# Optimization experiments

Hardware: AMD Instinct MI355X
Metric: run time of the kernel (lower is better)

## Reference

```python
import math
import jax, jax.numpy as jnp
import numpy as np

V = 32000   # vocab_size
NL = 8      # n_layer
NH = 16     # n_head
D = 1024    # n_embd
DH = D // NH
FF = 4 * D
B = 2
L = 1024
EPS = 1e-5


def setup_inputs() -> dict:
    key = jax.random.key(0)
    ks = jax.random.split(key, 10)
    std = 0.02  # matches nn.init.normal_(std=0.02)
    def nrm(k, shape):
        return jax.random.normal(k, shape, jnp.float32) * std
    return {
        "idx": jax.random.randint(ks[0], (B, L), 0, V),
        "tok_emb": nrm(ks[1], (V, D)),
        # per-layer params stacked on leading NL axis (scanned over)
        "ln1_w": jnp.ones((NL, D)), "ln1_b": jnp.zeros((NL, D)),
        "wq": nrm(ks[2], (NL, D, D)), "wk": nrm(ks[3], (NL, D, D)),
        "wv": nrm(ks[4], (NL, D, D)), "wo": nrm(ks[5], (NL, D, D)),
        "ln2_w": jnp.ones((NL, D)), "ln2_b": jnp.zeros((NL, D)),
        "w1": nrm(ks[6], (NL, D, FF)), "b1": jnp.zeros((NL, FF)),
        "w2": nrm(ks[7], (NL, FF, D)), "b2": jnp.zeros((NL, D)),
        "lnf_w": jnp.ones((D,)), "lnf_b": jnp.zeros((D,)),
        "lm_head": nrm(ks[8], (D, V)),
    }


def _sinusoidal_pe(seq_len, dim):
    pos = jnp.arange(seq_len, dtype=jnp.float32)[:, None]
    div = jnp.exp(jnp.arange(0, dim, 2, dtype=jnp.float32) * (-math.log(10000.0) / dim))
    pe = jnp.zeros((seq_len, dim), jnp.float32)
    pe = pe.at[:, 0::2].set(jnp.sin(pos * div))
    pe = pe.at[:, 1::2].set(jnp.cos(pos * div))
    return pe


def _ln(x, w, b):
    m = x.mean(-1, keepdims=True)
    v = ((x - m) ** 2).mean(-1, keepdims=True)
    return (x - m) * jax.lax.rsqrt(v + EPS) * w + b


def reference(idx, tok_emb, ln1_w, ln1_b, wq, wk, wv, wo,
              ln2_w, ln2_b, w1, b1, w2, b2, lnf_w, lnf_b, lm_head):
    b, l = idx.shape
    x = tok_emb[idx] + _sinusoidal_pe(l, tok_emb.shape[1])[None]  # [B,L,D]
    causal = jnp.tril(jnp.ones((l, l), bool))
    scale = 1.0 / math.sqrt(DH)

    def block(x, p):
        l1w, l1b, Wq, Wk, Wv, Wo, l2w, l2b, W1, B1, W2, B2 = p
        h = _ln(x, l1w, l1b)
        def heads(W):  # [B,L,D] -> [B,H,L,DH]
            return (h @ W).reshape(b, l, NH, DH).transpose(0, 2, 1, 3)
        q, k, v = heads(Wq), heads(Wk), heads(Wv)
        att = jnp.einsum('bhqd,bhkd->bhqk', q, k) * scale
        att = jnp.where(causal, att, -jnp.inf)
        att = jax.nn.softmax(att, axis=-1)
        y = jnp.einsum('bhqk,bhkd->bhqd', att, v)
        y = y.transpose(0, 2, 1, 3).reshape(b, l, -1)
        x = x + y @ Wo
        h2 = _ln(x, l2w, l2b)
        x = x + jax.nn.gelu(h2 @ W1 + B1, approximate=False) @ W2 + B2
        return x, None

    x, _ = jax.lax.scan(
        block, x, (ln1_w, ln1_b, wq, wk, wv, wo, ln2_w, ln2_b, w1, b1, w2, b2))
    x = _ln(x, lnf_w, lnf_b)
    return x @ lm_head  # [B,L,V] logits
```

## Files before the change

### kernel.cpp

```cpp
#include <hip/hip_runtime.h>
#include <math.h>

typedef unsigned short u16;
typedef __bf16 bfx8 __attribute__((ext_vector_type(8)));
typedef float f32x4 __attribute__((ext_vector_type(4)));

#define NLAYER  8
#define NHEAD   16
#define DMODEL  1024
#define DHEAD   64
#define DFF     4096
#define NB      2
#define SEQ     1024
#define NVOCAB  32000
#define NTOK    (NB*SEQ)
#define EPSLN   1e-5f
#define VCHUNK  6400
#define NSPLIT  2

__device__ __forceinline__ float bf2f(u16 u) {
  union { unsigned int i; float f; } x; x.i = ((unsigned int)u) << 16; return x.f;
}
__device__ __forceinline__ u16 f2bf(float f) {
  unsigned int x = __float_as_uint(f);
  x += 0x7fffu + ((x >> 16) & 1u);
  return (u16)(x >> 16);
}

#if defined(__has_builtin)
#if __has_builtin(__builtin_amdgcn_global_load_lds)
#define HAVE_GLL 1
#endif
#endif

__device__ __forceinline__ void gll16(const void* g, void* lds_base, int lane) {
#ifdef HAVE_GLL
  __builtin_amdgcn_global_load_lds((const __attribute__((address_space(1))) unsigned int*)g,
                                   (__attribute__((address_space(3))) unsigned int*)lds_base,
                                   16, 0, 0);
  (void)lane;
#else
  *(uint4*)((char*)lds_base + lane * 16) = *(const uint4*)g;
#endif
}

enum { EPI_QKV = 0, EPI_GELU_BIAS = 1, EPI_RESID = 2, EPI_RESID_BIAS = 3, EPI_LOGITS = 4 };

template <int EPI, int BM>
__global__ __launch_bounds__(256) void gemm_bt(
    const u16* __restrict__ A, const u16* __restrict__ Bt,
    const float* __restrict__ bias, u16* __restrict__ outb,
    float* __restrict__ outf, int M, int N, int K, int ldc)
{
  constexpr int ARND = BM / 64;
  constexpr int MF = BM / 32;
  constexpr int ABYTES = BM * 32 * 2;
  constexpr int BBYTES = 128 * 32 * 2;
  __shared__ __align__(16) u16 sA[2][BM * 32];
  __shared__ __align__(16) u16 sB[2][128 * 32];

  const int tid  = threadIdx.x;
  const int w    = tid >> 6;
  const int lane = tid & 63;
  const int l16  = lane & 15;
  const int hi   = lane >> 4;
  const int wm   = w >> 1;
  const int wn   = w & 1;

  const int nwg = gridDim.x;
  const int MB  = M / BM;
  const int orig = blockIdx.x;
  const int xcd = orig & 7, li = orig >> 3;
  const int q = nwg >> 3, r = nwg & 7;
  const int work = (xcd < r ? xcd * (q + 1) : r * (q + 1) + (xcd - r) * q) + li;
  const int m0 = (work % MB) * BM;
  const int n0 = (work / MB) * 128;

  const int srow = lane >> 2;
  const int su   = lane & 3;

  const u16* gA[ARND]; const u16* gB[2];
  int laOff[ARND]; int lbOff[2];
#pragma unroll
  for (int r2 = 0; r2 < ARND; r2++) {
    const int row = r2 * 64 + w * 16 + srow;
    const int gu = su ^ ((row >> 1) & 3);
    gA[r2] = A + (size_t)(m0 + row) * K + gu * 8;
    laOff[r2] = (r2 * 64 + w * 16) * 64;
  }
#pragma unroll
  for (int r2 = 0; r2 < 2; r2++) {
    const int row = r2 * 64 + w * 16 + srow;
    const int gu = su ^ ((row >> 1) & 3);
    gB[r2] = Bt + (size_t)(n0 + row) * K + gu * 8;
    lbOff[r2] = (r2 * 64 + w * 16) * 64;
  }

  f32x4 acc[MF][4];
#pragma unroll
  for (int i = 0; i < MF; i++)
#pragma unroll
    for (int j = 0; j < 4; j++)
#pragma unroll
      for (int r2 = 0; r2 < 4; r2++) acc[i][j][r2] = 0.0f;

#pragma unroll
  for (int r2 = 0; r2 < ARND; r2++) { gll16(gA[r2], (char*)sA[0] + laOff[r2], lane); gA[r2] += 32; }
#pragma unroll
  for (int r2 = 0; r2 < 2; r2++)    { gll16(gB[r2], (char*)sB[0] + lbOff[r2], lane); gB[r2] += 32; }
  __syncthreads();

  const int NT = K >> 5;
  int cur = 0;
  for (int t = 0; t < NT; ++t) {
    if (t + 1 < NT) {
      char* nA = (char*)sA[0] + (cur ^ 1) * ABYTES;
      char* nB = (char*)sB[0] + (cur ^ 1) * BBYTES;
#pragma unroll
      for (int r2 = 0; r2 < ARND; r2++) { gll16(gA[r2], nA + laOff[r2], lane); gA[r2] += 32; }
#pragma unroll
      for (int r2 = 0; r2 < 2; r2++)    { gll16(gB[r2], nB + lbOff[r2], lane); gB[r2] += 32; }
    }

    const char* cA = (const char*)sA[0] + cur * ABYTES;
    const char* cB = (const char*)sB[0] + cur * BBYTES;
    bfx8 aF[MF], bF[4];
#pragma unroll
    for (int i = 0; i < MF; i++) {
      const int row = wm * (BM / 2) + i * 16 + l16;
      aF[i] = *(const bfx8*)(cA + row * 64 + ((hi ^ ((row >> 1) & 3)) << 4));
    }
#pragma unroll
    for (int j = 0; j < 4; j++) {
      const int row = wn * 64 + j * 16 + l16;
      bF[j] = *(const bfx8*)(cB + row * 64 + ((hi ^ ((row >> 1) & 3)) << 4));
    }
#pragma unroll
    for (int i = 0; i < MF; i++)
#pragma unroll
      for (int j = 0; j < 4; j++)
        acc[i][j] = __builtin_amdgcn_mfma_f32_16x16x32_bf16(aF[i], bF[j], acc[i][j], 0, 0, 0);
    __syncthreads();
    cur ^= 1;
  }

  const int rbase = m0 + wm * (BM / 2);
  const int cbase = n0 + wn * 64;
#pragma unroll
  for (int i = 0; i < MF; i++) {
#pragma unroll
    for (int j = 0; j < 4; j++) {
      const int gcol = cbase + j * 16 + l16;
      float bv = 0.0f;
      if constexpr (EPI == EPI_GELU_BIAS || EPI == EPI_RESID_BIAS) bv = bias[gcol];
#pragma unroll
      for (int r2 = 0; r2 < 4; r2++) {
        const int grow = rbase + i * 16 + hi * 4 + r2;
        float v = acc[i][j][r2];
        const size_t oi = (size_t)grow * ldc + gcol;
        if constexpr (EPI == EPI_QKV) {
          outb[oi] = f2bf(v);
        } else if constexpr (EPI == EPI_GELU_BIAS) {
          v += bv;
          v = 0.5f * v * (1.0f + erff(v * 0.70710678118654752f));
          outb[oi] = f2bf(v);
        } else if constexpr (EPI == EPI_RESID) {
          outf[oi] += v;
        } else if constexpr (EPI == EPI_RESID_BIAS) {
          outf[oi] += v + bv;
        } else {
          outf[oi] = v;
        }
      }
    }
  }
}

__global__ __launch_bounds__(256) void ln_kernel(
    const float* __restrict__ x, const float* __restrict__ w,
    const float* __restrict__ b, u16* __restrict__ out)
{
  const int row = blockIdx.x;
  const int tid = threadIdx.x;
  const float* xr = x + (size_t)row * DMODEL;
  float4 v = *(const float4*)(xr + tid * 4);
  __shared__ float sbuf[4], qbuf[4];
  float s = v.x + v.y + v.z + v.w;
  float ss = v.x * v.x + v.y * v.y + v.z * v.z + v.w * v.w;
#pragma unroll
  for (int o = 32; o > 0; o >>= 1) { s += __shfl_xor(s, o, 64); ss += __shfl_xor(ss, o, 64); }
  if ((tid & 63) == 0) { sbuf[tid >> 6] = s; qbuf[tid >> 6] = ss; }
  __syncthreads();
  const float mean = (sbuf[0] + sbuf[1] + sbuf[2] + sbuf[3]) * (1.0f / DMODEL);
  const float ex2  = (qbuf[0] + qbuf[1] + qbuf[2] + qbuf[3]) * (1.0f / DMODEL);
  const float rstd = rsqrtf(ex2 - mean * mean + EPSLN);
  const int c = tid * 4;
  float dv[4] = {v.x - mean, v.y - mean, v.z - mean, v.w - mean};
#pragma unroll
  for (int e = 0; e < 4; e++)
    out[(size_t)row * DMODEL + c + e] = f2bf(dv[e] * rstd * w[c + e] + b[c + e]);
}

__global__ __launch_bounds__(256) void embed_kernel(
    const int* __restrict__ idx, const float* __restrict__ tok, float* __restrict__ x)
{
  const int row = blockIdx.x;
  const int l = row & (SEQ - 1);
  const int t = idx[row];
  const int d = threadIdx.x * 4;
#pragma unroll
  for (int e = 0; e < 4; e++) {
    const int dd = d + e;
    const float freq = expf((float)(dd & ~1) * (-9.210340371976184f / (float)DMODEL));
    const float ang = (float)l * freq;
    const float pe = (dd & 1) ? cosf(ang) : sinf(ang);
    x[(size_t)row * DMODEL + dd] = tok[(size_t)t * DMODEL + dd] + pe;
  }
}

__device__ __forceinline__ void transpose64_body(
    const float* __restrict__ in, u16* __restrict__ out,
    int rows, int cols, int c0, int r0)
{
  __shared__ float tile[64][65];
  const int lx = threadIdx.x & 15, ly = threadIdx.x >> 4;
#pragma unroll
  for (int ii = 0; ii < 4; ii++) {
    const int rr = ly + ii * 16;
    const float4 v = *(const float4*)&in[(size_t)(r0 + rr) * cols + c0 + lx * 4];
    tile[rr][lx * 4 + 0] = v.x;
    tile[rr][lx * 4 + 1] = v.y;
    tile[rr][lx * 4 + 2] = v.z;
    tile[rr][lx * 4 + 3] = v.w;
  }
  __syncthreads();
  const int sx = threadIdx.x & 31, sy = threadIdx.x >> 5;
#pragma unroll
  for (int ii = 0; ii < 8; ii++) {
    const int cc = sy + ii * 8;
    const unsigned int a = f2bf(tile[sx * 2][cc]);
    const unsigned int b = f2bf(tile[sx * 2 + 1][cc]);
    *(unsigned int*)&out[(size_t)(c0 + cc) * rows + r0 + sx * 2] = a | (b << 16);
  }
}

__global__ __launch_bounds__(256) void transpose64_b(
    const float* __restrict__ in, u16* __restrict__ out, int rows, int cols)
{
  transpose64_body(in, out, rows, cols, blockIdx.x * 64, blockIdx.y * 64);
}

__global__ __launch_bounds__(256) void transpose6_kernel(
    const float* __restrict__ wq, const float* __restrict__ wk,
    const float* __restrict__ wv, const float* __restrict__ wo,
    const float* __restrict__ w1, const float* __restrict__ w2,
    u16* __restrict__ wT)
{
  const size_t dd = (size_t)DMODEL * DMODEL, dff = (size_t)DMODEL * DFF;
  const int t = blockIdx.x;
  const float* in; u16* out; int rows, cols, cx, cy;
  if (t < 1024) {
    const int mat = t >> 8, tl = t & 255;
    in = (mat == 0) ? wq : (mat == 1) ? wk : (mat == 2) ? wv : wo;
    out = wT + (size_t)mat * dd; rows = DMODEL; cols = DMODEL;
    cx = tl & 15; cy = tl >> 4;
  } else if (t < 2048) {
    const int tl = t - 1024;
    in = w1; out = wT + 4 * dd; rows = DMODEL; cols = DFF;
    cx = tl & 63; cy = tl >> 6;
  } else {
    const int tl = t - 2048;
    in = w2; out = wT + 4 * dd + dff; rows = DFF; cols = DMODEL;
    cx = tl & 15; cy = tl >> 4;
  }
  transpose64_body(in, out, rows, cols, cx * 64, cy * 64);
}

__global__ __launch_bounds__(256) void vtrans_kernel(
    const u16* __restrict__ qkv, u16* __restrict__ vt)
{
  __shared__ u16 tile[32][33];
  const int bh = blockIdx.z;
  const int b = bh >> 4, hh = bh & 15;
  const int l0 = blockIdx.x * 32, d0 = blockIdx.y * 32;
  const int tx = threadIdx.x & 31, ty = threadIdx.x >> 5;
#pragma unroll
  for (int i = ty; i < 32; i += 8)
    tile[i][tx] = qkv[(size_t)(b * SEQ + l0 + i) * (3 * DMODEL) + 2 * DMODEL + hh * DHEAD + d0 + tx];
  __syncthreads();
#pragma unroll
  for (int i = ty; i < 32; i += 8)
    vt[(size_t)(bh * DHEAD + d0 + i) * SEQ + l0 + tx] = tile[tx][i];
}

__device__ __forceinline__ int plds_byte(int row, int col) {
  return row * 128 + ((((col >> 3) ^ (row & 7)) << 3) + (col & 7)) * 2;
}

__global__ __launch_bounds__(64) void attn_partial(
    const u16* __restrict__ qkv, const u16* __restrict__ vt,
    float* __restrict__ opart, float* __restrict__ lpart)
{
  __shared__ __align__(16) u16 p_lds[32 * 64];
  const int lane = threadIdx.x;
  const int l16 = lane & 15, hi = lane >> 4;
  const int qt = blockIdx.x, hh = blockIdx.y;
  const int b = blockIdx.z >> 1, sp = blockIdx.z & 1;
  const int q0 = qt * 32;
  const int T = (q0 + 95) >> 6;
  const int t_lo = (T * sp) >> 1;
  const int t_hi = (T * (sp + 1)) >> 1;

  const u16* qptr = qkv;
  const u16* kptr = qkv + DMODEL;
  const size_t rs3 = 3 * DMODEL;
  const size_t hoff = (size_t)hh * DHEAD;

  bfx8 aQ[2][2];
#pragma unroll
  for (int mt = 0; mt < 2; mt++)
#pragma unroll
    for (int kf = 0; kf < 2; kf++)
      aQ[mt][kf] = *(const bfx8*)&qptr[(size_t)(b * SEQ + q0 + mt * 16 + l16) * rs3 + hoff + kf * 32 + hi * 8];

  f32x4 o[2][4];
  float ssum[2][4];
#pragma unroll
  for (int mt = 0; mt < 2; mt++)
#pragma unroll
    for (int r = 0; r < 4; r++) ssum[mt][r] = 0.0f;
#pragma unroll
  for (int mt = 0; mt < 2; mt++)
#pragma unroll
    for (int dt = 0; dt < 4; dt++)
#pragma unroll
      for (int r = 0; r < 4; r++) o[mt][dt][r] = 0.0f;

  for (int kt = t_lo; kt < t_hi; kt++) {
    const int k0 = kt * 64;
    const bool diag = (kt == T - 1);

    bfx8 bK[4][2];
#pragma unroll
    for (int nt = 0; nt < 4; nt++)
#pragma unroll
      for (int kf = 0; kf < 2; kf++)
        bK[nt][kf] = *(const bfx8*)&kptr[(size_t)(b * SEQ + k0 + nt * 16 + l16) * rs3 + hoff + kf * 32 + hi * 8];

    f32x4 s[2][4];
#pragma unroll
    for (int mt = 0; mt < 2; mt++)
#pragma unroll
      for (int nt = 0; nt < 4; nt++) {
#pragma unroll
        for (int r = 0; r < 4; r++) s[mt][nt][r] = 0.0f;
        s[mt][nt] = __builtin_amdgcn_mfma_f32_16x16x32_bf16(aQ[mt][0], bK[nt][0], s[mt][nt], 0, 0, 0);
        s[mt][nt] = __builtin_amdgcn_mfma_f32_16x16x32_bf16(aQ[mt][1], bK[nt][1], s[mt][nt], 0, 0, 0);
      }

#pragma unroll
    for (int mt = 0; mt < 2; mt++) {
#pragma unroll
      for (int r = 0; r < 4; r++) {
        const int row_l = mt * 16 + hi * 4 + r;
        const int qrow = q0 + row_l;
        float p[4], rsum = 0.0f;
#pragma unroll
        for (int nt = 0; nt < 4; nt++) {
          const float sv = s[mt][nt][r] * 0.125f;
          const bool mask = diag && (k0 + nt * 16 + l16 > qrow);
          p[nt] = mask ? 0.0f : __expf(sv);
          rsum += p[nt];
        }
#pragma unroll
        for (int t = 1; t < 16; t <<= 1) rsum += __shfl_xor(rsum, t, 64);
        ssum[mt][r] += rsum;
#pragma unroll
        for (int nt = 0; nt < 4; nt++)
          *(u16*)((char*)p_lds + plds_byte(row_l, nt * 16 + l16)) = f2bf(p[nt]);
      }
    }
    __syncthreads();

    bfx8 pa[2][2];
#pragma unroll
    for (int mt = 0; mt < 2; mt++) {
      const int row = mt * 16 + l16;
#pragma unroll
      for (int kf = 0; kf < 2; kf++)
        pa[mt][kf] = *(const bfx8*)((const char*)p_lds + row * 128 + (((kf * 4 + hi) ^ (row & 7)) << 4));
    }
    bfx8 bV[4][2];
    const size_t vbase = (size_t)(b * NHEAD + hh) * DHEAD * SEQ;
#pragma unroll
    for (int dt = 0; dt < 4; dt++)
#pragma unroll
      for (int kf = 0; kf < 2; kf++)
        bV[dt][kf] = *(const bfx8*)&vt[vbase + (size_t)(dt * 16 + l16) * SEQ + k0 + kf * 32 + hi * 8];
#pragma unroll
    for (int mt = 0; mt < 2; mt++)
#pragma unroll
      for (int dt = 0; dt < 4; dt++) {
        o[mt][dt] = __builtin_amdgcn_mfma_f32_16x16x32_bf16(pa[mt][0], bV[dt][0], o[mt][dt], 0, 0, 0);
        o[mt][dt] = __builtin_amdgcn_mfma_f32_16x16x32_bf16(pa[mt][1], bV[dt][1], o[mt][dt], 0, 0, 0);
      }
    __syncthreads();
  }

  const size_t pbase = (((size_t)sp * NB + b) * NHEAD + hh) * SEQ + q0;
#pragma unroll
  for (int mt = 0; mt < 2; mt++) {
#pragma unroll
    for (int r = 0; r < 4; r++) {
      const int row_l = mt * 16 + hi * 4 + r;
      const size_t rg = pbase + row_l;
      if (l16 == 0) lpart[rg] = ssum[mt][r];
#pragma unroll
      for (int dt = 0; dt < 4; dt++)
        opart[rg * DHEAD + dt * 16 + l16] = o[mt][dt][r];
    }
  }
}

__global__ __launch_bounds__(256) void attn_combine(
    const float* __restrict__ opart, const float* __restrict__ lpart,
    u16* __restrict__ y)
{
  const int row = blockIdx.x;
  const int b = row >> 10;
  const int l = row & (SEQ - 1);
  const int t = threadIdx.x;
  const int hh = t >> 4;
  const int d0 = (t & 15) * 4;
  const size_t base = ((size_t)b * NHEAD + hh) * SEQ + l;
  const size_t stride = (size_t)NB * NHEAD * SEQ;
  float wsum = 0.0f;
  float4 acc = make_float4(0.f, 0.f, 0.f, 0.f);
#pragma unroll
  for (int i = 0; i < NSPLIT; i++) {
    wsum += lpart[base + i * stride];
    const float4 ov = *(const float4*)&opart[(base + i * stride) * DHEAD + d0];
    acc.x += ov.x; acc.y += ov.y; acc.z += ov.z; acc.w += ov.w;
  }
  const float dn = 1.0f / wsum;
  u16* yp = y + (size_t)row * DMODEL + hh * DHEAD + d0;
  yp[0] = f2bf(acc.x * dn);
  yp[1] = f2bf(acc.y * dn);
  yp[2] = f2bf(acc.z * dn);
  yp[3] = f2bf(acc.w * dn);
}

extern "C" void kernel_launch(void* const* d_in, const int* in_sizes, int n_in,
                              void* d_out, int out_size, void* d_ws, size_t ws_size,
                              hipStream_t stream)
{
  (void)in_sizes; (void)n_in; (void)out_size;
  const int*   idx  = (const int*)d_in[0];
  const float* tok  = (const float*)d_in[1];
  const float* ln1w = (const float*)d_in[2];
  const float* ln1b = (const float*)d_in[3];
  const float* wq   = (const float*)d_in[4];
  const float* wk   = (const float*)d_in[5];
  const float* wv   = (const float*)d_in[6];
  const float* wo   = (const float*)d_in[7];
  const float* ln2w = (const float*)d_in[8];
  const float* ln2b = (const float*)d_in[9];
  const float* w1   = (const float*)d_in[10];
  const float* b1   = (const float*)d_in[11];
  const float* w2   = (const float*)d_in[12];
  const float* b2   = (const float*)d_in[13];
  const float* lnfw = (const float*)d_in[14];
  const float* lnfb = (const float*)d_in[15];
  const float* lmh  = (const float*)d_in[16];
  float* out = (float*)d_out;

  char* ws = (char*)d_ws;
  size_t off = 0;
  auto alloc = [&](size_t bytes) -> void* {
    void* p = ws + off;
    off += (bytes + 255) & ~(size_t)255;
    return p;
  };
  float* x  = (float*)alloc((size_t)NTOK * DMODEL * 4);
  u16* h    = (u16*)alloc((size_t)NTOK * DMODEL * 2);
  u16* qkv  = (u16*)alloc((size_t)NTOK * 3 * DMODEL * 2);
  u16* vtb  = (u16*)alloc((size_t)NTOK * DMODEL * 2);
  u16* yb   = (u16*)alloc((size_t)NTOK * DMODEL * 2);
  u16* ffb  = (u16*)alloc((size_t)NTOK * DFF * 2);
  float* opart = (float*)alloc((size_t)NSPLIT * NB * NHEAD * SEQ * DHEAD * 4);
  float* lpart = (float*)alloc((size_t)NSPLIT * NB * NHEAD * SEQ * 4);

  const size_t dd = (size_t)DMODEL * DMODEL, dff = (size_t)DMODEL * DFF;
  const size_t perLayerElems = 4 * dd + 2 * dff;
  const size_t wT_bytes = perLayerElems * 2;
  const size_t lmhT_bytes = (size_t)NVOCAB * DMODEL * 2;

  u16* wT = (u16*)alloc(wT_bytes);
  const bool full_lmh = (off + lmhT_bytes) <= ws_size;
  u16* lmhT = full_lmh ? (u16*)alloc(lmhT_bytes) : nullptr;

  embed_kernel<<<NTOK, 256, 0, stream>>>(idx, tok, x);

  const int gQKV = (3 * DMODEL / 128) * (NTOK / 128);
  const int gFF1 = (DFF / 128) * (NTOK / 128);
  const int gD64 = (DMODEL / 128) * (NTOK / 64);

  u16* wqT = wT;
  u16* woT = wT + 3 * dd;
  u16* w1T = wT + 4 * dd;
  u16* w2T = w1T + dff;

  for (int layer = 0; layer < NLAYER; layer++) {
    transpose6_kernel<<<3072, 256, 0, stream>>>(
        wq + layer * dd, wk + layer * dd, wv + layer * dd, wo + layer * dd,
        w1 + layer * dff, w2 + layer * dff, wT);

    ln_kernel<<<NTOK, 256, 0, stream>>>(x, ln1w + layer * DMODEL, ln1b + layer * DMODEL, h);
    gemm_bt<EPI_QKV, 128><<<gQKV, 256, 0, stream>>>(h, wqT, nullptr, qkv, nullptr,
                                                    NTOK, 3 * DMODEL, DMODEL, 3 * DMODEL);
    vtrans_kernel<<<dim3(SEQ / 32, DHEAD / 32, NB * NHEAD), 256, 0, stream>>>(qkv, vtb);
    attn_partial<<<dim3(SEQ / 32, NHEAD, NB * NSPLIT), 64, 0, stream>>>(
        qkv, vtb, opart, lpart);
    attn_combine<<<NB * SEQ, 256, 0, stream>>>(opart, lpart, yb);
    gemm_bt<EPI_RESID, 64><<<gD64, 256, 0, stream>>>(yb, woT, nullptr, nullptr, x,
                                                     NTOK, DMODEL, DMODEL, DMODEL);
    ln_kernel<<<NTOK, 256, 0, stream>>>(x, ln2w + layer * DMODEL, ln2b + layer * DMODEL, h);
    gemm_bt<EPI_GELU_BIAS, 128><<<gFF1, 256, 0, stream>>>(h, w1T, b1 + (size_t)layer * DFF, ffb,
                                                          nullptr, NTOK, DFF, DMODEL, DFF);
    gemm_bt<EPI_RESID_BIAS, 64><<<gD64, 256, 0, stream>>>(ffb, w2T, b2 + (size_t)layer * DMODEL,
                                                          nullptr, x, NTOK, DMODEL, DFF, DMODEL);
  }

  ln_kernel<<<NTOK, 256, 0, stream>>>(x, lnfw, lnfb, h);

  if (full_lmh) {
    transpose64_b<<<dim3(NVOCAB / 64, DMODEL / 64), 256, 0, stream>>>(lmh, lmhT, DMODEL, NVOCAB);
    const int gLM = (NVOCAB / 128) * (NTOK / 128);
    gemm_bt<EPI_LOGITS, 128><<<gLM, 256, 0, stream>>>(
        h, lmhT, nullptr, nullptr, out, NTOK, NVOCAB, DMODEL, NVOCAB);
  } else {
    for (int c = 0; c < NVOCAB / VCHUNK; c++) {
      transpose64_b<<<dim3(VCHUNK / 64, DMODEL / 64), 256, 0, stream>>>(
          lmh + (size_t)c * VCHUNK, wT, DMODEL, NVOCAB);
      gemm_bt<EPI_LOGITS, 128><<<(VCHUNK / 128) * (NTOK / 128), 256, 0, stream>>>(
          h, wT, nullptr, nullptr, out + (size_t)c * VCHUNK,
          NTOK, VCHUNK, DMODEL, NVOCAB);
    }
  }
}
```

Baseline: 1.887 ms.

## Triple-buffer GEMM LDS tiles with explicit vmcnt waits for deeper prefetch

Moves the bf16 GEMM main loop from double-buffered to triple-buffered LDS staging. Loads run two K-tiles ahead, and explicit s_waitcnt vmcnt counts wait only for the tile about to be consumed, with raw s_barrier calls between stages. The aim is to hide global-to-LDS latency better. The cost is more LDS per block, which may lower occupancy, two barriers per iteration, and fragile hand-counted vmcnt values that assume a fixed number of loads per stage.

```diff
diff --git a/kernel.cpp b/kernel.cpp
--- a/kernel.cpp
+++ b/kernel.cpp
@@ -44,6 +44,15 @@
 #endif
 }
 
+template <int N>
+__device__ __forceinline__ void wait_vmcnt() {
+  if constexpr (N == 0) asm volatile("s_waitcnt vmcnt(0)" ::: "memory");
+  else if constexpr (N == 3) asm volatile("s_waitcnt vmcnt(3)" ::: "memory");
+  else if constexpr (N == 4) asm volatile("s_waitcnt vmcnt(4)" ::: "memory");
+  else if constexpr (N == 6) asm volatile("s_waitcnt vmcnt(6)" ::: "memory");
+  else if constexpr (N == 8) asm volatile("s_waitcnt vmcnt(8)" ::: "memory");
+}
+
 enum { EPI_QKV = 0, EPI_GELU_BIAS = 1, EPI_RESID = 2, EPI_RESID_BIAS = 3, EPI_LOGITS = 4 };
 
 template <int EPI, int BM>
@@ -54,10 +63,11 @@
 {
   constexpr int ARND = BM / 64;
   constexpr int MF = BM / 32;
+  constexpr int L = ARND + 2;
   constexpr int ABYTES = BM * 32 * 2;
   constexpr int BBYTES = 128 * 32 * 2;
-  __shared__ __align__(16) u16 sA[2][BM * 32];
-  __shared__ __align__(16) u16 sB[2][128 * 32];
+  __shared__ __align__(16) u16 sA[3][BM * 32];
+  __shared__ __align__(16) u16 sB[3][128 * 32];
 
   const int tid  = threadIdx.x;
   const int w    = tid >> 6;
@@ -108,22 +118,35 @@
   for (int r2 = 0; r2 < ARND; r2++) { gll16(gA[r2], (char*)sA[0] + laOff[r2], lane); gA[r2] += 32; }
 #pragma unroll
   for (int r2 = 0; r2 < 2; r2++)    { gll16(gB[r2], (char*)sB[0] + lbOff[r2], lane); gB[r2] += 32; }
-  __syncthreads();
+#pragma unroll
+  for (int r2 = 0; r2 < ARND; r2++) { gll16(gA[r2], (char*)sA[1] + laOff[r2], lane); gA[r2] += 32; }
+#pragma unroll
+  for (int r2 = 0; r2 < 2; r2++)    { gll16(gB[r2], (char*)sB[1] + lbOff[r2], lane); gB[r2] += 32; }
+  __builtin_amdgcn_sched_barrier(0);
 
   const int NT = K >> 5;
-  int cur = 0;
+  int cbuf = 0;
   for (int t = 0; t < NT; ++t) {
-    if (t + 1 < NT) {
-      char* nA = (char*)sA[0] + (cur ^ 1) * ABYTES;
-      char* nB = (char*)sB[0] + (cur ^ 1) * BBYTES;
+    if (t + 2 < NT) {
+      int nb = cbuf + 2; if (nb >= 3) nb -= 3;
+      char* nA = (char*)sA[0] + nb * ABYTES;
+      char* nB = (char*)sB[0] + nb * BBYTES;
 #pragma unroll
       for (int r2 = 0; r2 < ARND; r2++) { gll16(gA[r2], nA + laOff[r2], lane); gA[r2] += 32; }
 #pragma unroll
       for (int r2 = 0; r2 < 2; r2++)    { gll16(gB[r2], nB + lbOff[r2], lane); gB[r2] += 32; }
-    }
-
-    const char* cA = (const char*)sA[0] + cur * ABYTES;
-    const char* cB = (const char*)sB[0] + cur * BBYTES;
+      __builtin_amdgcn_sched_barrier(0);
+    }
+
+    if (t + 2 < NT)      wait_vmcnt<2 * L>();
+    else if (t + 1 < NT) wait_vmcnt<L>();
+    else                 wait_vmcnt<0>();
+    __builtin_amdgcn_sched_barrier(0);
+    __builtin_amdgcn_s_barrier();
+    __builtin_amdgcn_sched_barrier(0);
+
+    const char* cA = (const char*)sA[0] + cbuf * ABYTES;
+    const char* cB = (const char*)sB[0] + cbuf * BBYTES;
     bfx8 aF[MF], bF[4];
 #pragma unroll
     for (int i = 0; i < MF; i++) {
@@ -140,8 +163,11 @@
 #pragma unroll
       for (int j = 0; j < 4; j++)
         acc[i][j] = __builtin_amdgcn_mfma_f32_16x16x32_bf16(aF[i], bF[j], acc[i][j], 0, 0, 0);
-    __syncthreads();
-    cur ^= 1;
+
+    __builtin_amdgcn_sched_barrier(0);
+    __builtin_amdgcn_s_barrier();
+    __builtin_amdgcn_sched_barrier(0);
+    cbuf = (cbuf + 1 == 3) ? 0 : cbuf + 1;
   }
 
   const int rbase = m0 + wm * (BM / 2);
```

After: 1.951 ms. 3.4% more time.
